# Kernel tuning notes

Measured on AMD Instinct MI355X. Metric: run time of the kernel, lower is better.

Reference implementation:

```python
import jax, jax.numpy as jnp
import numpy as np

N = 6144
IN_F = 256
OUT_F = 64
ALPHA = 0.2  # leaky relu slope
NEG_INF = -9e15
ADJ_DENSITY = 0.01


def setup_inputs() -> dict:
    key = jax.random.key(0)
    kx, ka, kw, kat, ks, ke = jax.random.split(key, 6)
    x = jax.random.normal(kx, (N, IN_F), dtype=jnp.float32)
    adj = (jax.random.uniform(ka, (N, N)) < ADJ_DENSITY).astype(jnp.float32)
    adj = adj.at[jnp.arange(N), jnp.arange(N)].set(0.0)
    # xavier-uniform-ish init scale (gain 1.414)
    def xavier(k, shape):
        fan_in, fan_out = shape[0], shape[1]
        lim = 1.414 * np.sqrt(6.0 / (fan_in + fan_out))
        return jax.random.uniform(k, shape, minval=-lim, maxval=lim, dtype=jnp.float32)
    W = xavier(kw, (IN_F, OUT_F))
    a = xavier(kat, (2 * OUT_F, 1))
    W_si = xavier(ks, (1, 1))
    W_ei = xavier(ke, (1, 1))
    return {"x": x, "adj": adj, "W": W, "a": a, "W_si": W_si, "W_ei": W_ei}


def reference(x, adj, W, a, W_si, W_ei):
    # h: [N, F_out]
    h = x @ W
    # additive GAT score: e[i,j] = leakyrelu(Wh1[i] + Wh2[j])
    Wh1 = h @ a[:OUT_F, :]           # [N, 1]
    Wh2 = h @ a[OUT_F:, :]           # [N, 1]
    e = jax.nn.leaky_relu(Wh1 + Wh2.T, negative_slope=ALPHA)  # [N, N]
    # adjacency-power topology bias
    adj2 = adj @ adj
    adj3 = adj2 @ adj
    adj_w = adj + adj2 + adj3
    adj_w = adj_w.at[jnp.arange(N), jnp.arange(N)].set(0.0)
    e = jnp.abs(W_ei) * e + jnp.abs(W_si) * adj_w
    # masked softmax over neighbors (row-wise)
    scores = jnp.where(adj > 0, e, NEG_INF)
    attention = jax.nn.softmax(scores, axis=1)
    # dropout omitted (eval mode / training=False)
    h_prime = attention @ h
    return jax.nn.elu(h_prime)
```

## Files before the change

### kernel.cpp

```cpp
#include <hip/hip_runtime.h>
#include <math.h>

#define N 6144
#define MAXD 128
#define NWORDS 96
#define NW32 192

typedef unsigned long long u64;
typedef unsigned int u32;
typedef unsigned char u8;
typedef float f4 __attribute__((ext_vector_type(4)));


__device__ __forceinline__ int a_addr(int j) {
    int vdx = (j & ~255) | ((j & 3) << 6) | ((j >> 2) & 63);
    return (((vdx >> 2) & 7) << 10) | ((vdx >> 5) << 2) | (vdx & 3);
}

#define FA(s, c, a, b, ci) { u32 _t = (a) ^ (b); (s) = _t ^ (ci); (c) = ((a) & (b)) | ((ci) & _t); }

template <int START>
__device__ __forceinline__ void badd_from(u32* p, u32 cy) {
    #pragma unroll
    for (int q = START; q < 6; ++q) { u32 x = p[q] & cy; p[q] ^= cy; cy = x; }
    p[6] ^= cy;
}

__device__ __forceinline__ void csa15(u32* p, const u32* x) {
    u32 s0,c0,s1,c1,s2,c2,s3,c3,s4,c4;
    FA(s0,c0, x[0], x[1], x[2]);
    FA(s1,c1, x[3], x[4], x[5]);
    FA(s2,c2, x[6], x[7], x[8]);
    FA(s3,c3, x[9], x[10], x[11]);
    FA(s4,c4, x[12], x[13], x[14]);
    u32 t0,d0,u0,d1;
    FA(t0,d0, s0, s1, s2);
    FA(u0,d1, s3, s4, t0);
    u32 e0,f0,e1,f1,e2,f2;
    FA(e0,f0, c0, c1, c2);
    FA(e1,f1, c3, c4, d0);
    FA(e2,f2, e0, e1, d1);
    u32 g0,h0;
    FA(g0,h0, f0, f1, f2);
    badd_from<0>(p, u0);
    badd_from<1>(p, e2);
    badd_from<2>(p, g0);
    badd_from<3>(p, h0);
}

__device__ __forceinline__ u64 bit_transpose64(u64 x, int lane) {
    const u64 masks[6] = {0xAAAAAAAAAAAAAAAAull, 0xCCCCCCCCCCCCCCCCull,
                          0xF0F0F0F0F0F0F0F0ull, 0xFF00FF00FF00FF00ull,
                          0xFFFF0000FFFF0000ull, 0xFFFFFFFF00000000ull};
    #pragma unroll
    for (int k = 0; k < 6; ++k) {
        int s = 1 << k;
        u64 m = masks[k];
        u64 y = (u64)__shfl_xor((long long)x, s, 64);
        x = (lane & s) ? ((x & m) | ((y & m) >> s))
                       : ((x & ~m) | ((y & ~m) << s));
    }
    return x;
}

__global__ __launch_bounds__(256) void k_gemm_h(
    const float* __restrict__ x, const float* __restrict__ W,
    const float* __restrict__ a,
    float* __restrict__ h, float* __restrict__ Wh1, float* __restrict__ Wh2)
{
    __shared__ float Wl[256 * 64];
    int t = threadIdx.x;
    #pragma unroll
    for (int c = 0; c < 64; ++c) Wl[c * 256 + t] = W[c * 256 + t];
    __syncthreads();

    int w = t >> 6, lane = t & 63;
    int i0 = blockIdx.x * 32 + w * 8;
    const float* xr = x + (long)i0 * 256;

    float acc[8] = {0.f, 0.f, 0.f, 0.f, 0.f, 0.f, 0.f, 0.f};
    for (int k0 = 0; k0 < 256; k0 += 4) {
        float4 xv[8];
        #pragma unroll
        for (int r = 0; r < 8; ++r)
            xv[r] = *(const float4*)(xr + (long)r * 256 + k0);
        #pragma unroll
        for (int kk = 0; kk < 4; ++kk) {
            float wv = Wl[(k0 + kk) * 64 + lane];
            #pragma unroll
            for (int r = 0; r < 8; ++r) {
                float xs = (kk == 0) ? xv[r].x : (kk == 1) ? xv[r].y
                         : (kk == 2) ? xv[r].z : xv[r].w;
                acc[r] = fmaf(xs, wv, acc[r]);
            }
        }
    }

    #pragma unroll
    for (int r = 0; r < 8; ++r) {
        int i = i0 + r;
        h[(long)i * 64 + lane] = acc[r];
        float s1 = acc[r] * a[lane];
        float s2 = acc[r] * a[64 + lane];
        #pragma unroll
        for (int off = 32; off; off >>= 1) {
            s1 += __shfl_xor(s1, off, 64);
            s2 += __shfl_xor(s2, off, 64);
        }
        if (lane == 0) { Wh1[i] = s1; Wh2[i] = s2; }
    }
}

__global__ __launch_bounds__(256) void k_build(
    const float* __restrict__ adj,
    u64* __restrict__ rowbits, int* __restrict__ row_cnt, int* __restrict__ row_list)
{
    int i = blockIdx.x;
    int t = threadIdx.x, w = t >> 6, lane = t & 63;
    __shared__ int wtot[4];

    const f4* ar = (const f4*)(adj + (long)i * N) + (w * 6) * 64;

    f4 v[6];
    #pragma unroll
    for (int c = 0; c < 6; ++c)
        v[c] = __builtin_nontemporal_load(ar + c * 64 + lane);

    u64 m[6][4];
    #pragma unroll
    for (int c = 0; c < 6; ++c) {
        m[c][0] = __ballot(v[c].x != 0.0f);
        m[c][1] = __ballot(v[c].y != 0.0f);
        m[c][2] = __ballot(v[c].z != 0.0f);
        m[c][3] = __ballot(v[c].w != 0.0f);
    }

    int tot = 0;
    #pragma unroll
    for (int c = 0; c < 6; ++c) {
        #pragma unroll
        for (int p = 0; p < 4; ++p) tot += __popcll(m[c][p]);
    }
    if (lane == 0) wtot[w] = tot;
    __syncthreads();
    int base = 0;
    #pragma unroll
    for (int q = 0; q < 4; ++q) if (q < w) base += wtot[q];

    u64* rb = rowbits + (long)i * NWORDS + w * 24;
    #pragma unroll
    for (int c = 0; c < 6; ++c) {
        #pragma unroll
        for (int p = 0; p < 4; ++p) {
            u64 mm = m[c][p];
            if (lane == 0) rb[c * 4 + p] = mm;
            if ((mm >> lane) & 1ull) {
                int rank = __popcll(mm & ((1ull << lane) - 1ull));
                int s = base + rank;
                int j = (w * 6 + c) * 256 + (lane << 2) + p;
                if (s < MAXD) row_list[(long)i * MAXD + s] = j;
            }
            base += __popcll(mm);
        }
    }
    if (t == 0) {
        int tt = wtot[0] + wtot[1] + wtot[2] + wtot[3];
        row_cnt[i] = tt < 127 ? tt : 127;
    }
}

__global__ __launch_bounds__(256) void k_trans(
    const u64* __restrict__ rowbits, u64* __restrict__ colbits)
{
    int w = threadIdx.x >> 6, lane = threadIdx.x & 63;
    int tile = blockIdx.x * 4 + w;
    int tr = tile / 96, tc = tile - tr * 96;
    u64 x = rowbits[(long)(tr * 64 + lane) * NWORDS + tc];
    x = bit_transpose64(x, lane);
    colbits[(long)(tc * 64 + lane) * NWORDS + tr] = x;
}

__global__ __launch_bounds__(256) void k_collist(
    const u64* __restrict__ colbits,
    int* __restrict__ col_cnt, int* __restrict__ col_list)
{
    int w = threadIdx.x >> 6, lane = threadIdx.x & 63;
    int v = blockIdx.x * 4 + w;
    int j = (v & ~255) | ((v & 63) << 2) | ((v >> 6) & 3);

    u64 w0 = 0, w1 = 0;
    if (lane < 48) {
        const u64* p2 = colbits + (long)v * NWORDS + lane * 2;
        w0 = p2[0]; w1 = p2[1];
    }
    int pc = __popcll(w0) + __popcll(w1);
    int incl = pc;
    #pragma unroll
    for (int off = 1; off < 64; off <<= 1) {
        int y = __shfl_up(incl, off, 64);
        if (lane >= off) incl += y;
    }
    int excl = incl - pc;
    int total = __shfl(incl, 63, 64);
    if (lane == 0) col_cnt[j] = total;

    int* cl = col_list + (long)j * MAXD;
    int s = excl;
    int ibase = lane * 128;
    while (w0) {
        int b = __ffsll((long long)w0) - 1; w0 &= w0 - 1;
        if (s < MAXD) cl[s] = ibase + b;
        ++s;
    }
    ibase += 64;
    while (w1) {
        int b = __ffsll((long long)w1) - 1; w1 &= w1 - 1;
        if (s < MAXD) cl[s] = ibase + b;
        ++s;
    }
}

__global__ __launch_bounds__(256) void k_attn(
    const float* __restrict__ h, const float* __restrict__ Wh1, const float* __restrict__ Wh2,
    const u64* __restrict__ rowbits,
    const int* __restrict__ row_cnt, const int* __restrict__ row_list,
    const int* __restrict__ col_cnt, const int* __restrict__ col_list,
    const float* __restrict__ W_si, const float* __restrict__ W_ei,
    float* __restrict__ out)
{
    __shared__ u32 adj2p[8 * 256];
    __shared__ int nbr[MAXD];
    __shared__ int ccbuf[MAXD];
    __shared__ float lrbuf[MAXD];
    __shared__ float ebuf[MAXD];
    __shared__ float part[256];
    __shared__ float sh_max, sh_sum;

    int i = blockIdx.x;
    int t = threadIdx.x, w = t >> 6, lane = t & 63;
    int deg = row_cnt[i];
    deg = deg < 127 ? deg : 127;

    if (deg == 0) {
        float acc = 0.f;
        for (int r = w; r < N; r += 4) acc += h[(long)r * 64 + lane];
        part[t] = acc;
        __syncthreads();
        if (w == 0) {
            float s = part[lane] + part[64 + lane] + part[128 + lane] + part[192 + lane];
            s *= (1.0f / N);
            out[(long)i * 64 + lane] = s > 0.f ? s : expm1f(s);
        }
        return;
    }

    float aWei = fabsf(W_ei[0]);
    float aWsi = fabsf(W_si[0]);

    if (t < deg) {
        int j = row_list[(long)i * MAXD + t];
        nbr[t] = j;
        int cc = col_cnt[j];
        ccbuf[t] = cc < MAXD ? cc : MAXD;
        float z = Wh1[i] + Wh2[j];
        lrbuf[t] = aWei * (z > 0.f ? z : 0.2f * z);
    }

    if (t < NW32) {
        const u32* rb32 = (const u32*)rowbits;
        const int* rl = row_list + (long)i * MAXD;
        u32 p[7] = {0,0,0,0,0,0,0};

        int m = 0;
        for (; m + 15 <= deg; m += 15) {
            u32 x[15];
            #pragma unroll
            for (int q = 0; q < 15; ++q) {
                int j = rl[m + q];
                x[q] = rb32[(long)j * NW32 + t];
            }
            csa15(p, x);
        }
        if (m < deg) {
            u32 x[15];
            #pragma unroll
            for (int q = 0; q < 15; ++q) {
                int mq = m + q;
                int j = rl[mq < deg ? mq : 0];
                u32 vv = rb32[(long)j * NW32 + t];
                x[q] = (mq < deg) ? vv : 0u;
            }
            csa15(p, x);
        }

        #pragma unroll
        for (int g = 0; g < 8; ++g) {
            u32 acc = 0;
            #pragma unroll
            for (int pl = 0; pl < 7; ++pl) {
                u32 nib = (p[pl] >> (4 * g)) & 0xFu;
                acc += (nib * (0x00204081u << pl)) & (0x01010101u << pl);
            }
            adj2p[g * 256 + t] = acc;
        }
    }
    __syncthreads();

    const u8* adj2b = (const u8*)adj2p;

    {
        int g = t >> 3, sub = t & 7;
        for (int e = g; e < deg; e += 32) {
            int j = nbr[e];
            int cc = ccbuf[e];
            const int* cl = col_list + (long)j * MAXD;
            u32 a3 = 0;
            for (int q = sub; q < cc; q += 8) {
                int k = cl[q];
                a3 += (u32)adj2b[a_addr(k)];
            }
            a3 += __shfl_xor(a3, 1, 64);
            a3 += __shfl_xor(a3, 2, 64);
            a3 += __shfl_xor(a3, 4, 64);
            if (sub == 0) {
                u32 a2 = (u32)adj2b[a_addr(j)];
                ebuf[e] = lrbuf[e] + aWsi * (float)(1u + a2 + a3);
            }
        }
    }
    __syncthreads();

    if (w == 0) {
        float v = -3.4e38f;
        for (int idx = lane; idx < deg; idx += 64) v = fmaxf(v, ebuf[idx]);
        #pragma unroll
        for (int off = 32; off; off >>= 1) v = fmaxf(v, __shfl_xor(v, off, 64));
        if (lane == 0) sh_max = v;
    }
    __syncthreads();
    if (t < deg) ebuf[t] = expf(ebuf[t] - sh_max);
    __syncthreads();
    if (w == 0) {
        float s = 0.f;
        for (int idx = lane; idx < deg; idx += 64) s += ebuf[idx];
        #pragma unroll
        for (int off = 32; off; off >>= 1) s += __shfl_xor(s, off, 64);
        if (lane == 0) sh_sum = s;
    }
    __syncthreads();

    float acc0 = 0.f, acc1 = 0.f;
    int e = w;
    for (; e + 4 < deg; e += 8) {
        acc0 = fmaf(ebuf[e],     h[(long)nbr[e]     * 64 + lane], acc0);
        acc1 = fmaf(ebuf[e + 4], h[(long)nbr[e + 4] * 64 + lane], acc1);
    }
    if (e < deg)
        acc0 = fmaf(ebuf[e], h[(long)nbr[e] * 64 + lane], acc0);
    part[t] = acc0 + acc1;
    __syncthreads();
    if (w == 0) {
        float s = part[lane] + part[64 + lane] + part[128 + lane] + part[192 + lane];
        s /= sh_sum;
        out[(long)i * 64 + lane] = s > 0.f ? s : expm1f(s);
    }
}

extern "C" void kernel_launch(void* const* d_in, const int* in_sizes, int n_in,
                              void* d_out, int out_size, void* d_ws, size_t ws_size,
                              hipStream_t stream) {
    const float* x    = (const float*)d_in[0];
    const float* adj  = (const float*)d_in[1];
    const float* W    = (const float*)d_in[2];
    const float* a    = (const float*)d_in[3];
    const float* W_si = (const float*)d_in[4];
    const float* W_ei = (const float*)d_in[5];
    float* out = (float*)d_out;

    char* ws = (char*)d_ws;
    size_t off = 0;
    auto alloc = [&](size_t bytes) -> void* {
        void* p = ws + off;
        off += (bytes + 255) & ~(size_t)255;
        return p;
    };
    u64*   rowbits  = (u64*)  alloc((size_t)N * NWORDS * sizeof(u64));
    u64*   colbits  = (u64*)  alloc((size_t)N * NWORDS * sizeof(u64));
    float* h        = (float*)alloc((size_t)N * 64 * sizeof(float));
    float* Wh1      = (float*)alloc((size_t)N * sizeof(float));
    float* Wh2      = (float*)alloc((size_t)N * sizeof(float));
    int*   row_cnt  = (int*)  alloc((size_t)N * sizeof(int));
    int*   row_list = (int*)  alloc((size_t)N * MAXD * sizeof(int));
    int*   col_cnt  = (int*)  alloc((size_t)N * sizeof(int));
    int*   col_list = (int*)  alloc((size_t)N * MAXD * sizeof(int));

    k_gemm_h <<<N / 32, 256, 0, stream>>>(x, W, a, h, Wh1, Wh2);
    k_build  <<<N, 256, 0, stream>>>(adj, rowbits, row_cnt, row_list);
    k_trans  <<<(96 * 96) / 4, 256, 0, stream>>>(rowbits, colbits);
    k_collist<<<N / 4, 256, 0, stream>>>(colbits, col_cnt, col_list);
    k_attn   <<<N, 256, 0, stream>>>(h, Wh1, Wh2, rowbits, row_cnt, row_list,
                                     col_cnt, col_list, W_si, W_ei, out);
}
```

Measured before the change: 306.2 us.

## Split adjacency bitmask build from list construction and merge row/col list kernels

The per-row build kernel, which read a full adjacency row and also wrote the neighbor list, is replaced by a lightweight bit-extraction kernel on a 2D grid. Each thread in that kernel does one vector load and one ballot. Row neighbor lists are now built from the row bitmasks inside a combined list kernel that also builds the column lists. The aim is more memory-level parallelism on the large adjacency read and no serial list-writing tail on that bandwidth-bound pass. The cost is an extra read of the row bitmasks. Row lists now come out in bit-index order rather than column order, and the row count is no longer clamped to 127.

```diff
diff --git a/kernel.cpp b/kernel.cpp
--- a/kernel.cpp
+++ b/kernel.cpp
@@ -111,61 +111,23 @@
     }
 }
 
-__global__ __launch_bounds__(256) void k_build(
-    const float* __restrict__ adj,
-    u64* __restrict__ rowbits, int* __restrict__ row_cnt, int* __restrict__ row_list)
-{
-    int i = blockIdx.x;
+__global__ __launch_bounds__(256) void k_bits(
+    const float* __restrict__ adj, u64* __restrict__ rowbits)
+{
+    int q = blockIdx.x;
+    int i = blockIdx.y;
     int t = threadIdx.x, w = t >> 6, lane = t & 63;
-    __shared__ int wtot[4];
-
-    const f4* ar = (const f4*)(adj + (long)i * N) + (w * 6) * 64;
-
-    f4 v[6];
-    #pragma unroll
-    for (int c = 0; c < 6; ++c)
-        v[c] = __builtin_nontemporal_load(ar + c * 64 + lane);
-
-    u64 m[6][4];
-    #pragma unroll
-    for (int c = 0; c < 6; ++c) {
-        m[c][0] = __ballot(v[c].x != 0.0f);
-        m[c][1] = __ballot(v[c].y != 0.0f);
-        m[c][2] = __ballot(v[c].z != 0.0f);
-        m[c][3] = __ballot(v[c].w != 0.0f);
-    }
-
-    int tot = 0;
-    #pragma unroll
-    for (int c = 0; c < 6; ++c) {
-        #pragma unroll
-        for (int p = 0; p < 4; ++p) tot += __popcll(m[c][p]);
-    }
-    if (lane == 0) wtot[w] = tot;
-    __syncthreads();
-    int base = 0;
-    #pragma unroll
-    for (int q = 0; q < 4; ++q) if (q < w) base += wtot[q];
-
-    u64* rb = rowbits + (long)i * NWORDS + w * 24;
-    #pragma unroll
-    for (int c = 0; c < 6; ++c) {
-        #pragma unroll
-        for (int p = 0; p < 4; ++p) {
-            u64 mm = m[c][p];
-            if (lane == 0) rb[c * 4 + p] = mm;
-            if ((mm >> lane) & 1ull) {
-                int rank = __popcll(mm & ((1ull << lane) - 1ull));
-                int s = base + rank;
-                int j = (w * 6 + c) * 256 + (lane << 2) + p;
-                if (s < MAXD) row_list[(long)i * MAXD + s] = j;
-            }
-            base += __popcll(mm);
-        }
-    }
-    if (t == 0) {
-        int tt = wtot[0] + wtot[1] + wtot[2] + wtot[3];
-        row_cnt[i] = tt < 127 ? tt : 127;
+
+    const f4* ar = (const f4*)(adj + (long)i * N + q * 1024);
+    f4 v = __builtin_nontemporal_load(ar + t);
+
+    u64 m0 = __ballot(v.x != 0.0f);
+    u64 m1 = __ballot(v.y != 0.0f);
+    u64 m2 = __ballot(v.z != 0.0f);
+    u64 m3 = __ballot(v.w != 0.0f);
+    if (lane == 0) {
+        u64* rb = rowbits + (long)i * NWORDS + (q * 4 + w) * 4;
+        rb[0] = m0; rb[1] = m1; rb[2] = m2; rb[3] = m3;
     }
 }
 
@@ -180,17 +142,20 @@
     colbits[(long)(tc * 64 + lane) * NWORDS + tr] = x;
 }
 
-__global__ __launch_bounds__(256) void k_collist(
-    const u64* __restrict__ colbits,
+__global__ __launch_bounds__(256) void k_lists(
+    const u64* __restrict__ rowbits, const u64* __restrict__ colbits,
+    int* __restrict__ row_cnt, int* __restrict__ row_list,
     int* __restrict__ col_cnt, int* __restrict__ col_list)
 {
     int w = threadIdx.x >> 6, lane = threadIdx.x & 63;
-    int v = blockIdx.x * 4 + w;
-    int j = (v & ~255) | ((v & 63) << 2) | ((v >> 6) & 3);
+    int idx = blockIdx.x * 4 + w;
+    bool isRow = idx < N;
+    int r = isRow ? idx : idx - N;
+    const u64* src = (isRow ? rowbits : colbits) + (long)r * NWORDS;
 
     u64 w0 = 0, w1 = 0;
     if (lane < 48) {
-        const u64* p2 = colbits + (long)v * NWORDS + lane * 2;
+        const u64* p2 = src + lane * 2;
         w0 = p2[0]; w1 = p2[1];
     }
     int pc = __popcll(w0) + __popcll(w1);
@@ -202,21 +167,44 @@
     }
     int excl = incl - pc;
     int total = __shfl(incl, 63, 64);
-    if (lane == 0) col_cnt[j] = total;
-
-    int* cl = col_list + (long)j * MAXD;
-    int s = excl;
-    int ibase = lane * 128;
-    while (w0) {
-        int b = __ffsll((long long)w0) - 1; w0 &= w0 - 1;
-        if (s < MAXD) cl[s] = ibase + b;
-        ++s;
-    }
-    ibase += 64;
-    while (w1) {
-        int b = __ffsll((long long)w1) - 1; w1 &= w1 - 1;
-        if (s < MAXD) cl[s] = ibase + b;
-        ++s;
+
+    if (isRow) {
+        if (lane == 0) row_cnt[r] = total;
+        int* dst = row_list + (long)r * MAXD;
+        int s = excl;
+        int v = lane * 128;
+        while (w0) {
+            int b = __ffsll((long long)w0) - 1; w0 &= w0 - 1;
+            int vv = v + b;
+            int j = (vv & ~255) | ((vv & 63) << 2) | ((vv >> 6) & 3);
+            if (s < MAXD) dst[s] = j;
+            ++s;
+        }
+        v += 64;
+        while (w1) {
+            int b = __ffsll((long long)w1) - 1; w1 &= w1 - 1;
+            int vv = v + b;
+            int j = (vv & ~255) | ((vv & 63) << 2) | ((vv >> 6) & 3);
+            if (s < MAXD) dst[s] = j;
+            ++s;
+        }
+    } else {
+        int j = (r & ~255) | ((r & 63) << 2) | ((r >> 6) & 3);
+        if (lane == 0) col_cnt[j] = total;
+        int* dst = col_list + (long)j * MAXD;
+        int s = excl;
+        int ibase = lane * 128;
+        while (w0) {
+            int b = __ffsll((long long)w0) - 1; w0 &= w0 - 1;
+            if (s < MAXD) dst[s] = ibase + b;
+            ++s;
+        }
+        ibase += 64;
+        while (w1) {
+            int b = __ffsll((long long)w1) - 1; w1 &= w1 - 1;
+            if (s < MAXD) dst[s] = ibase + b;
+            ++s;
+        }
     }
 }
 
@@ -394,10 +382,11 @@
     int*   col_cnt  = (int*)  alloc((size_t)N * sizeof(int));
     int*   col_list = (int*)  alloc((size_t)N * MAXD * sizeof(int));
 
-    k_gemm_h <<<N / 32, 256, 0, stream>>>(x, W, a, h, Wh1, Wh2);
-    k_build  <<<N, 256, 0, stream>>>(adj, rowbits, row_cnt, row_list);
-    k_trans  <<<(96 * 96) / 4, 256, 0, stream>>>(rowbits, colbits);
-    k_collist<<<N / 4, 256, 0, stream>>>(colbits, col_cnt, col_list);
-    k_attn   <<<N, 256, 0, stream>>>(h, Wh1, Wh2, rowbits, row_cnt, row_list,
-                                     col_cnt, col_list, W_si, W_ei, out);
-}
+    k_gemm_h<<<N / 32, 256, 0, stream>>>(x, W, a, h, Wh1, Wh2);
+    k_bits  <<<dim3(6, N), 256, 0, stream>>>(adj, rowbits);
+    k_trans <<<(96 * 96) / 4, 256, 0, stream>>>(rowbits, colbits);
+    k_lists <<<(2 * N) / 4, 256, 0, stream>>>(rowbits, colbits,
+                                              row_cnt, row_list, col_cnt, col_list);
+    k_attn  <<<N, 256, 0, stream>>>(h, Wh1, Wh2, rowbits, row_cnt, row_list,
+                                    col_cnt, col_list, W_si, W_ei, out);
+}
```

Result: no change. 307.2 us (+0.3%).
